# Performance work log

Measured on AMD Instinct MI355X. Metric: run time of the kernel, lower is better.

## Reference

```python
import jax, jax.numpy as jnp
import numpy as np

V, L, D, C = 50000, 512, 300, 128
KS = (3, 4, 5)
B = 64


def setup_inputs() -> dict:
    key = jax.random.key(0)
    ks = jax.random.split(key, 12)
    inp = {
        "x": jax.random.randint(ks[0], (B, L), 0, V),
        "embed_w": jax.random.normal(ks[1], (V, D), jnp.float32) * 0.1,
        "conv_w": jax.random.normal(ks[2], (C, D), jnp.float32) * 0.05,
        "conv_b": jax.random.normal(ks[3], (C,), jnp.float32) * 0.05,
        "fc3_w": jax.random.normal(ks[4], (L - 3,), jnp.float32) * 0.04,
        "fc3_b": jax.random.normal(ks[5], (1,), jnp.float32) * 0.04,
        "fc4_w": jax.random.normal(ks[6], (L - 4,), jnp.float32) * 0.04,
        "fc4_b": jax.random.normal(ks[7], (1,), jnp.float32) * 0.04,
        "fc5_w": jax.random.normal(ks[8], (L - 5,), jnp.float32) * 0.04,
        "fc5_b": jax.random.normal(ks[9], (1,), jnp.float32) * 0.04,
        "fc_w": jax.random.normal(ks[10], (C, C * len(KS)), jnp.float32) * 0.05,
        "fc_b": jax.random.normal(ks[11], (C,), jnp.float32) * 0.05,
    }
    return inp


def reference(x, embed_w, conv_w, conv_b, fc3_w, fc3_b, fc4_w, fc4_b,
              fc5_w, fc5_b, fc_w, fc_b):
    # Embedding lookup: [B, L, D]
    emb = embed_w[x]
    # Exclusive prefix sum over the sequence dim (O(L) sliding sums).
    cs = jnp.concatenate(
        [jnp.zeros_like(emb[:, :1]), jnp.cumsum(emb, axis=1)], axis=1)  # [B, L+1, D]
    fcs = ((fc3_w, fc3_b), (fc4_w, fc4_b), (fc5_w, fc5_b))
    outs = []
    for k, (wk, bk) in zip(KS, fcs):
        # Window i sums tokens i..i+k-1; only L-k windows (range(L-k) in original).
        win = cs[:, k:L] - cs[:, :L - k]                      # [B, L-k, D]
        # conv_sim: dot each window-sum against C label vectors (kernel (1, D)).
        sim = jnp.einsum('bld,cd->bcl', win, conv_w) + conv_b[None, :, None]
        # Dropout is identity in eval; fcs[k]: Linear(L-k, 1) shared across channels.
        outs.append(jnp.einsum('bcl,l->bc', sim, wk) + bk)    # [B, C]
    h = jnp.concatenate(outs, axis=1)                          # [B, C*3]
    return h @ fc_w.T + fc_b                                   # [B, C]
```

## Files before the change

### kernel.cpp

```cpp
#include <hip/hip_runtime.h>
#include <stdint.h>

#define BB 64
#define LL 512
#define DD 300
#define CC 128

#define OFF_HT (BB * 32 * 3 * DD)

__global__ __launch_bounds__(256) void k_gather(
    const int* __restrict__ x, const float* __restrict__ embed,
    const float* __restrict__ w3, const float* __restrict__ w4,
    const float* __restrict__ w5, float* __restrict__ Gpart) {
  const int b = blockIdx.x >> 4;
  const int tc = blockIdx.x & 15;
  const int tid = threadIdx.x;
  const int sub = tid >> 7;
  const int stid = tid & 127;

  __shared__ int sx[32];
  __shared__ float su[3][32];

  if (tid < 32) {
    const int t = tc * 32 + tid;
    sx[tid] = x[b * LL + t];
    const float* ws[3] = {w3, w4, w5};
#pragma unroll
    for (int kk = 0; kk < 3; ++kk) {
      const int k = kk + 3;
      int lo = t - k + 1; if (lo < 0) lo = 0;
      int hi = t; const int lim = LL - k - 1; if (hi > lim) hi = lim;
      float s = 0.f;
      for (int l = lo; l <= hi; ++l) s += ws[kk][l];
      su[kk][tid] = s;
    }
  }
  __syncthreads();

  float a0x = 0.f, a0y = 0.f, a1x = 0.f, a1y = 0.f, a2x = 0.f, a2y = 0.f;
  float c0x = 0.f, c0y = 0.f, c1x = 0.f, c1y = 0.f, c2x = 0.f, c2y = 0.f;
  const bool tail = stid < (DD / 2 - 128);

#pragma unroll
  for (int half = 0; half < 2; ++half) {
    const int base = sub * 16 + half * 8;
    float2 v[8], u[8];
#pragma unroll
    for (int i = 0; i < 8; ++i) {
      const float2* rp = (const float2*)(embed + (size_t)sx[base + i] * DD);
      v[i] = rp[stid];
    }
    if (tail) {
#pragma unroll
      for (int i = 0; i < 8; ++i) {
        const float2* rp = (const float2*)(embed + (size_t)sx[base + i] * DD);
        u[i] = rp[128 + stid];
      }
    }
#pragma unroll
    for (int i = 0; i < 8; ++i) {
      const int j = base + i;
      const float w0 = su[0][j], w1 = su[1][j], w2 = su[2][j];
      a0x += w0 * v[i].x; a0y += w0 * v[i].y;
      a1x += w1 * v[i].x; a1y += w1 * v[i].y;
      a2x += w2 * v[i].x; a2y += w2 * v[i].y;
      if (tail) {
        c0x += w0 * u[i].x; c0y += w0 * u[i].y;
        c1x += w1 * u[i].x; c1y += w1 * u[i].y;
        c2x += w2 * u[i].x; c2y += w2 * u[i].y;
      }
    }
  }

  const int p = tc * 2 + sub;
  float* Gp = Gpart + (size_t)(b * 32 + p) * (3 * DD);
  const int d0 = 2 * stid;
  Gp[0 * DD + d0] = a0x; Gp[0 * DD + d0 + 1] = a0y;
  Gp[1 * DD + d0] = a1x; Gp[1 * DD + d0 + 1] = a1y;
  Gp[2 * DD + d0] = a2x; Gp[2 * DD + d0 + 1] = a2y;
  if (tail) {
    const int d1 = 2 * (128 + stid);
    Gp[0 * DD + d1] = c0x; Gp[0 * DD + d1 + 1] = c0y;
    Gp[1 * DD + d1] = c1x; Gp[1 * DD + d1 + 1] = c1y;
    Gp[2 * DD + d1] = c2x; Gp[2 * DD + d1 + 1] = c2y;
  }
}

__global__ __launch_bounds__(256) void k_redsim(
    const float* __restrict__ Gpart, const float* __restrict__ conv_w,
    const float* __restrict__ conv_b,
    const float* __restrict__ w3, const float* __restrict__ b3,
    const float* __restrict__ w4, const float* __restrict__ b4,
    const float* __restrict__ w5, const float* __restrict__ b5,
    float* __restrict__ hT) {
  const int blk = blockIdx.x;
  const int b = blk / 3;
  const int kk = blk - b * 3;
  const int tid = threadIdx.x;
  const int sub = tid >> 7;
  const int stid = tid & 127;

  __shared__ float2 sGh[2][150];
  __shared__ float red[256];

  {
    const float2* base =
        (const float2*)Gpart + ((size_t)(b * 32 + sub * 16) * 3 + kk) * 150;
    const bool tail = stid < 22;
    float2 acc0 = {0.f, 0.f}, acc1 = {0.f, 0.f};
#pragma unroll
    for (int half = 0; half < 2; ++half) {
      float2 v[8], u[8];
#pragma unroll
      for (int i = 0; i < 8; ++i)
        v[i] = base[(size_t)(half * 8 + i) * 450 + stid];
      if (tail) {
#pragma unroll
        for (int i = 0; i < 8; ++i)
          u[i] = base[(size_t)(half * 8 + i) * 450 + 128 + stid];
      }
#pragma unroll
      for (int i = 0; i < 8; ++i) {
        acc0.x += v[i].x; acc0.y += v[i].y;
        if (tail) { acc1.x += u[i].x; acc1.y += u[i].y; }
      }
    }
    sGh[sub][stid] = acc0;
    if (tail) sGh[sub][128 + stid] = acc1;
  }

  const float* wk = (kk == 0) ? w3 : ((kk == 1) ? w4 : w5);
  const float* bk = (kk == 0) ? b3 : ((kk == 1) ? b4 : b5);
  {
    const int len = LL - (kk + 3);
    float s = (tid < len) ? wk[tid] : 0.f;
    if (tid + 256 < len) s += wk[tid + 256];
    red[tid] = s;
  }
  __syncthreads();
  for (int off = 128; off >= 1; off >>= 1) {
    if (tid < off) red[tid] += red[tid + off];
    __syncthreads();
  }
  const float Sk = red[0];
  const float bkv = bk[0];

  const int lane = tid & 63;
  const int wid = tid >> 6;
  for (int m = 0; m < 32; ++m) {
    const int cp = wid * 32 + m;
    const float2* cwp = (const float2*)(conv_w + cp * DD);
    float acc;
    {
      const float2 v = cwp[lane];
      const float2 g0 = sGh[0][lane], g1 = sGh[1][lane];
      acc = v.x * (g0.x + g1.x) + v.y * (g0.y + g1.y);
    }
    {
      const float2 v = cwp[lane + 64];
      const float2 g0 = sGh[0][lane + 64], g1 = sGh[1][lane + 64];
      acc += v.x * (g0.x + g1.x) + v.y * (g0.y + g1.y);
    }
    if (lane < 22) {
      const float2 v = cwp[lane + 128];
      const float2 g0 = sGh[0][lane + 128], g1 = sGh[1][lane + 128];
      acc += v.x * (g0.x + g1.x) + v.y * (g0.y + g1.y);
    }
#pragma unroll
    for (int off = 32; off >= 1; off >>= 1) acc += __shfl_down(acc, off, 64);
    if (lane == 0) {
      hT[b * (3 * CC) + kk * CC + cp] = acc + conv_b[cp] * Sk + bkv;
    }
  }
}

__global__ __launch_bounds__(256) void k_fc(
    const float* __restrict__ hT, const float* __restrict__ fcw,
    const float* __restrict__ fcb, float* __restrict__ out) {
  const int o = blockIdx.x * 4 + (threadIdx.x >> 6);
  const int lane = threadIdx.x & 63;
  const int b = o >> 7;
  const int c = o & 127;

  const float* fr = fcw + c * (3 * CC);
  const float* hr = hT + b * (3 * CC);
  float acc = 0.f;
#pragma unroll
  for (int s = 0; s < 6; ++s) acc += fr[s * 64 + lane] * hr[s * 64 + lane];
#pragma unroll
  for (int off = 32; off >= 1; off >>= 1) acc += __shfl_down(acc, off, 64);
  if (lane == 0) out[b * CC + c] = acc + fcb[c];
}

extern "C" void kernel_launch(void* const* d_in, const int* in_sizes, int n_in,
                              void* d_out, int out_size, void* d_ws,
                              size_t ws_size, hipStream_t stream) {
  const int* x = (const int*)d_in[0];
  const float* embed = (const float*)d_in[1];
  const float* conv_w = (const float*)d_in[2];
  const float* conv_b = (const float*)d_in[3];
  const float* fc3w = (const float*)d_in[4];
  const float* fc3b = (const float*)d_in[5];
  const float* fc4w = (const float*)d_in[6];
  const float* fc4b = (const float*)d_in[7];
  const float* fc5w = (const float*)d_in[8];
  const float* fc5b = (const float*)d_in[9];
  const float* fcw = (const float*)d_in[10];
  const float* fcb = (const float*)d_in[11];

  float* Gpart = (float*)d_ws;
  float* hT = (float*)d_ws + OFF_HT;

  k_gather<<<dim3(BB * 16), dim3(256), 0, stream>>>(x, embed, fc3w, fc4w,
                                                    fc5w, Gpart);
  k_redsim<<<dim3(BB * 3), dim3(256), 0, stream>>>(
      Gpart, conv_w, conv_b, fc3w, fc3b, fc4w, fc4b, fc5w, fc5b, hT);
  k_fc<<<dim3(2048), dim3(256), 0, stream>>>(hT, fcw, fcb, (float*)d_out);
}
```

Before: 146.1 us.

## Restructure reduce-sim kernel into 8 blocks per batch with float4 partial reduction

Replaces the per-(batch,k) reduce/similarity kernel with one that launches 8 blocks per batch. Each block reduces all 32 gather partials for all three k values with float4 loads, then computes 48 of the 384 output channels per block, 12 per wave. The fc weight sums now use a per-wave shuffle reduction in place of a shared-memory tree with many barriers. This raises parallelism and shortens each block's serial loop, but every block redundantly re-reduces the full partial buffer for its batch.

```diff
diff --git a/kernel.cpp b/kernel.cpp
--- a/kernel.cpp
+++ b/kernel.cpp
@@ -86,90 +86,81 @@
   }
 }
 
-__global__ __launch_bounds__(256) void k_redsim(
+__global__ __launch_bounds__(256) void k_redsim2(
     const float* __restrict__ Gpart, const float* __restrict__ conv_w,
     const float* __restrict__ conv_b,
     const float* __restrict__ w3, const float* __restrict__ b3,
     const float* __restrict__ w4, const float* __restrict__ b4,
     const float* __restrict__ w5, const float* __restrict__ b5,
     float* __restrict__ hT) {
-  const int blk = blockIdx.x;
-  const int b = blk / 3;
-  const int kk = blk - b * 3;
+  const int b = blockIdx.x >> 3;
+  const int g = blockIdx.x & 7;
   const int tid = threadIdx.x;
-  const int sub = tid >> 7;
-  const int stid = tid & 127;
-
-  __shared__ float2 sGh[2][150];
-  __shared__ float red[256];
-
-  {
-    const float2* base =
-        (const float2*)Gpart + ((size_t)(b * 32 + sub * 16) * 3 + kk) * 150;
-    const bool tail = stid < 22;
-    float2 acc0 = {0.f, 0.f}, acc1 = {0.f, 0.f};
-#pragma unroll
-    for (int half = 0; half < 2; ++half) {
-      float2 v[8], u[8];
-#pragma unroll
-      for (int i = 0; i < 8; ++i)
-        v[i] = base[(size_t)(half * 8 + i) * 450 + stid];
-      if (tail) {
-#pragma unroll
-        for (int i = 0; i < 8; ++i)
-          u[i] = base[(size_t)(half * 8 + i) * 450 + 128 + stid];
-      }
-#pragma unroll
-      for (int i = 0; i < 8; ++i) {
-        acc0.x += v[i].x; acc0.y += v[i].y;
-        if (tail) { acc1.x += u[i].x; acc1.y += u[i].y; }
-      }
-    }
-    sGh[sub][stid] = acc0;
-    if (tail) sGh[sub][128 + stid] = acc1;
-  }
-
-  const float* wk = (kk == 0) ? w3 : ((kk == 1) ? w4 : w5);
-  const float* bk = (kk == 0) ? b3 : ((kk == 1) ? b4 : b5);
-  {
-    const int len = LL - (kk + 3);
-    float s = (tid < len) ? wk[tid] : 0.f;
-    if (tid + 256 < len) s += wk[tid + 256];
-    red[tid] = s;
-  }
-  __syncthreads();
-  for (int off = 128; off >= 1; off >>= 1) {
-    if (tid < off) red[tid] += red[tid + off];
-    __syncthreads();
-  }
-  const float Sk = red[0];
-  const float bkv = bk[0];
-
   const int lane = tid & 63;
   const int wid = tid >> 6;
-  for (int m = 0; m < 32; ++m) {
-    const int cp = wid * 32 + m;
+
+  __shared__ __align__(16) float sG[3 * DD];
+  __shared__ float sSk[3], sbk[3];
+
+  if (tid < 225) {
+    const float4* gp = (const float4*)Gpart + (size_t)b * 32 * 225 + tid;
+    float4 acc = {0.f, 0.f, 0.f, 0.f};
+#pragma unroll
+    for (int p0 = 0; p0 < 32; p0 += 8) {
+      float4 v[8];
+#pragma unroll
+      for (int i = 0; i < 8; ++i) v[i] = gp[(size_t)(p0 + i) * 225];
+#pragma unroll
+      for (int i = 0; i < 8; ++i) {
+        acc.x += v[i].x; acc.y += v[i].y; acc.z += v[i].z; acc.w += v[i].w;
+      }
+    }
+    ((float4*)sG)[tid] = acc;
+  }
+
+  if (wid < 3) {
+    const float* wk = (wid == 0) ? w3 : ((wid == 1) ? w4 : w5);
+    const int len = LL - (wid + 3);
+    float s = 0.f;
+    for (int l = lane; l < len; l += 64) s += wk[l];
+#pragma unroll
+    for (int off = 32; off >= 1; off >>= 1) s += __shfl_down(s, off, 64);
+    if (lane == 0) {
+      sSk[wid] = s;
+      sbk[wid] = (wid == 0) ? b3[0] : ((wid == 1) ? b4[0] : b5[0]);
+    }
+  }
+  __syncthreads();
+
+  const float2* sG2 = (const float2*)sG;
+  const int j0 = g * 48 + wid * 12;
+#pragma unroll 2
+  for (int m = 0; m < 12; ++m) {
+    const int j = j0 + m;
+    const int kk = j >> 7;
+    const int cp = j & 127;
     const float2* cwp = (const float2*)(conv_w + cp * DD);
+    const float2* g2 = sG2 + kk * 150;
     float acc;
     {
       const float2 v = cwp[lane];
-      const float2 g0 = sGh[0][lane], g1 = sGh[1][lane];
-      acc = v.x * (g0.x + g1.x) + v.y * (g0.y + g1.y);
+      const float2 gg = g2[lane];
+      acc = v.x * gg.x + v.y * gg.y;
     }
     {
       const float2 v = cwp[lane + 64];
-      const float2 g0 = sGh[0][lane + 64], g1 = sGh[1][lane + 64];
-      acc += v.x * (g0.x + g1.x) + v.y * (g0.y + g1.y);
+      const float2 gg = g2[lane + 64];
+      acc += v.x * gg.x + v.y * gg.y;
     }
     if (lane < 22) {
       const float2 v = cwp[lane + 128];
-      const float2 g0 = sGh[0][lane + 128], g1 = sGh[1][lane + 128];
-      acc += v.x * (g0.x + g1.x) + v.y * (g0.y + g1.y);
+      const float2 gg = g2[lane + 128];
+      acc += v.x * gg.x + v.y * gg.y;
     }
 #pragma unroll
     for (int off = 32; off >= 1; off >>= 1) acc += __shfl_down(acc, off, 64);
     if (lane == 0) {
-      hT[b * (3 * CC) + kk * CC + cp] = acc + conv_b[cp] * Sk + bkv;
+      hT[b * (3 * CC) + j] = acc + conv_b[cp] * sSk[kk] + sbk[kk];
     }
   }
 }
@@ -213,7 +204,7 @@
 
   k_gather<<<dim3(BB * 16), dim3(256), 0, stream>>>(x, embed, fc3w, fc4w,
                                                     fc5w, Gpart);
-  k_redsim<<<dim3(BB * 3), dim3(256), 0, stream>>>(
+  k_redsim2<<<dim3(BB * 8), dim3(256), 0, stream>>>(
       Gpart, conv_w, conv_b, fc3w, fc3b, fc4w, fc4b, fc5w, fc5b, hT);
   k_fc<<<dim3(2048), dim3(256), 0, stream>>>(hT, fcw, fcb, (float*)d_out);
 }
```

Result: faster. 137.9 us (-5.6%).
